# Optimization experiments

Measured on AMD Instinct MI355X. Metric: run time of the kernel, lower is better.

The kernel has to match this reference:

```python
import jax, jax.numpy as jnp
import numpy as np

EMB = 1024
HEADS = 16
EPS = 1e-6


def setup_inputs() -> dict:
    key = jax.random.key(0)
    ks = jax.random.split(key, 12)
    B, S, D = 2, 2048, EMB
    scale = 1.0 / np.sqrt(D)
    inp = {
        "v": jax.random.normal(ks[0], (B, S, D), jnp.float32),
        "k": jax.random.normal(ks[1], (B, S, D), jnp.float32),
        "q": jax.random.normal(ks[2], (B, S, D), jnp.float32),
        "Wv": jax.random.normal(ks[3], (D, D), jnp.float32) * scale,
        "bv": jnp.zeros((D,), jnp.float32),
        "Wk": jax.random.normal(ks[4], (D, D), jnp.float32) * scale,
        "bk": jnp.zeros((D,), jnp.float32),
        "Wq": jax.random.normal(ks[5], (D, D), jnp.float32) * scale,
        "bq": jnp.zeros((D,), jnp.float32),
        "Wo": jax.random.normal(ks[6], (D, D), jnp.float32) * scale,
        "bo": jnp.zeros((D,), jnp.float32),
        "gamma": jnp.ones((D,), jnp.float32),
        "beta": jnp.zeros((D,), jnp.float32),
    }
    return inp


def reference(v, k, q, Wv, bv, Wk, bk, Wq, bq, Wo, bo, gamma, beta):
    B, S, D = q.shape
    H = HEADS
    d = D // H  # head depth

    def split_heads(x):  # [B,S,D] -> [B,H,S,d]
        return x.reshape(B, S, H, d).transpose(0, 2, 1, 3)

    V = split_heads(v @ Wv + bv)
    K = split_heads(k @ Wk + bk)
    Q = split_heads(q @ Wq + bq)

    # scaled dot-product attention (full score matrix, no mask)
    scores = jnp.einsum("bhqd,bhkd->bhqk", Q, K) / jnp.sqrt(jnp.float32(d))
    attn = jax.nn.softmax(scores, axis=-1)
    ctx = jnp.einsum("bhqk,bhkd->bhqd", attn, V)

    ctx = ctx.transpose(0, 2, 1, 3).reshape(B, S, D)
    out = ctx @ Wo + bo + q  # final dense + residual

    # LayerNormalization(epsilon=1e-6) over last axis
    mu = jnp.mean(out, axis=-1, keepdims=True)
    var = jnp.var(out, axis=-1, keepdims=True)
    return gamma * (out - mu) * jax.lax.rsqrt(var + EPS) + beta
```

## Files before the change

kernel.cpp:

```cpp
#include <hip/hip_runtime.h>
#include <hip/hip_bf16.h>
#include <math.h>

#define D_EMB 1024
#define NBATCH 2
#define SEQ 2048
#define NH 16
#define HDIM 64
#define MTOT (NBATCH*SEQ)

typedef unsigned short u16;
typedef __attribute__((ext_vector_type(8))) short bf16x8;
typedef __attribute__((ext_vector_type(4))) float f32x4;
typedef __attribute__((ext_vector_type(16))) float f32x16;
typedef __attribute__((ext_vector_type(4))) unsigned short u16x4;
typedef __attribute__((ext_vector_type(4))) unsigned int u32x4;

__device__ __forceinline__ u16 f2b(float f) {
  union { float f; unsigned u; } x; x.f = f;
  unsigned r = x.u + 0x7fffu + ((x.u >> 16) & 1u);
  return (u16)(r >> 16);
}

__device__ __forceinline__ void gld_lds16(const u16* g, u16* l) {
  __builtin_amdgcn_global_load_lds(
      (const __attribute__((address_space(1))) void*)g,
      (__attribute__((address_space(3))) void*)l, 16, 0, 0);
}

__global__ __launch_bounds__(256) void convert_qkv(
    const float* __restrict__ v, const float* __restrict__ k, const float* __restrict__ q,
    u16* __restrict__ vb, u16* __restrict__ kb, u16* __restrict__ qb) {
  int idx = blockIdx.x * 256 + threadIdx.x;
  float4 a;
  u16x4 o;
  a = ((const float4*)v)[idx];
  o.x = f2b(a.x); o.y = f2b(a.y); o.z = f2b(a.z); o.w = f2b(a.w);
  ((u16x4*)vb)[idx] = o;
  a = ((const float4*)k)[idx];
  o.x = f2b(a.x); o.y = f2b(a.y); o.z = f2b(a.z); o.w = f2b(a.w);
  ((u16x4*)kb)[idx] = o;
  a = ((const float4*)q)[idx];
  o.x = f2b(a.x); o.y = f2b(a.y); o.z = f2b(a.z); o.w = f2b(a.w);
  ((u16x4*)qb)[idx] = o;
}

__global__ __launch_bounds__(256) void transpose_w(
    const float* __restrict__ Wv, const float* __restrict__ Wk,
    const float* __restrict__ Wq, const float* __restrict__ Wo,
    u16* __restrict__ Wvt, u16* __restrict__ Wkt,
    u16* __restrict__ Wqt, u16* __restrict__ Wot) {
  __shared__ float tile[32][33];
  int z = blockIdx.z;
  const float* W = (z==0) ? Wv : (z==1) ? Wk : (z==2) ? Wq : Wo;
  u16* Wt = (z==0) ? Wvt : (z==1) ? Wkt : (z==2) ? Wqt : Wot;
  int tx = threadIdx.x, ty = threadIdx.y;
  int n0 = blockIdx.x * 32, k0 = blockIdx.y * 32;
#pragma unroll
  for (int i = 0; i < 4; ++i)
    tile[ty + i*8][tx] = W[(size_t)(k0 + ty + i*8) * D_EMB + n0 + tx];
  __syncthreads();
#pragma unroll
  for (int i = 0; i < 4; ++i)
    Wt[(size_t)(n0 + ty + i*8) * D_EMB + k0 + tx] = f2b(tile[tx][ty + i*8]);
}

__device__ __forceinline__ void gemm_loop(
    const u16* __restrict__ A, const u16* __restrict__ Bt,
    u16* lds_a, u16* lds_b, int bm, int bn, int wid, int lane,
    int wr, int wc, f32x4 acc[4][4]) {
#pragma unroll 1
  for (int kt = 0; kt < D_EMB/64; ++kt) {
    __syncthreads();
#pragma unroll
    for (int i = 0; i < 4; ++i) {
      int chunk = i*4 + wid;
      int row = chunk*8 + (lane >> 3);
      int slot = (lane & 7) ^ (row & 7);
      const u16* srcA = A + (size_t)(bm*128 + row) * D_EMB + kt*64 + slot*8;
      gld_lds16(srcA, lds_a + chunk*512);
      const u16* srcB = Bt + (size_t)(bn*128 + row) * D_EMB + kt*64 + slot*8;
      gld_lds16(srcB, lds_b + chunk*512);
    }
    __syncthreads();
#pragma unroll
    for (int st = 0; st < 2; ++st) {
      bf16x8 af[4], bfr[4];
#pragma unroll
      for (int mb = 0; mb < 4; ++mb) {
        int row = wr*64 + mb*16 + (lane & 15);
        int slot = (st*4 + (lane >> 4)) ^ (row & 7);
        af[mb] = *(const bf16x8*)(lds_a + row*64 + slot*8);
      }
#pragma unroll
      for (int nb = 0; nb < 4; ++nb) {
        int row = wc*64 + nb*16 + (lane & 15);
        int slot = (st*4 + (lane >> 4)) ^ (row & 7);
        bfr[nb] = *(const bf16x8*)(lds_b + row*64 + slot*8);
      }
#pragma unroll
      for (int mb = 0; mb < 4; ++mb)
#pragma unroll
        for (int nb = 0; nb < 4; ++nb)
          acc[mb][nb] = __builtin_amdgcn_mfma_f32_16x16x32_bf16(af[mb], bfr[nb], acc[mb][nb], 0, 0, 0);
    }
  }
}

__global__ __launch_bounds__(256) void gemm_qkv(
    const u16* __restrict__ vb, const u16* __restrict__ kb, const u16* __restrict__ qb,
    const u16* __restrict__ Wvt, const u16* __restrict__ Wkt, const u16* __restrict__ Wqt,
    const float* __restrict__ bv, const float* __restrict__ bk, const float* __restrict__ bq,
    u16* __restrict__ Vt, u16* __restrict__ Kh, u16* __restrict__ Qh) {
  __shared__ u16 lds_a[128*64];
  __shared__ u16 lds_b[128*64];
  int z = blockIdx.z;
  const u16* A  = (z==0) ? vb : (z==1) ? kb : qb;
  const u16* Bt = (z==0) ? Wvt : (z==1) ? Wkt : Wqt;
  const float* bias = (z==0) ? bv : (z==1) ? bk : bq;
  int tid = threadIdx.x, wid = tid >> 6, lane = tid & 63;
  int wr = wid >> 1, wc = wid & 1;
  int bm = blockIdx.y, bn = blockIdx.x;
  f32x4 acc[4][4];
#pragma unroll
  for (int i = 0; i < 4; ++i)
#pragma unroll
    for (int j = 0; j < 4; ++j) acc[i][j] = (f32x4){0.f,0.f,0.f,0.f};
  gemm_loop(A, Bt, lds_a, lds_b, bm, bn, wid, lane, wr, wc, acc);
  int g = lane >> 4, c = lane & 15;
#pragma unroll
  for (int mb = 0; mb < 4; ++mb) {
    int row0 = bm*128 + wr*64 + mb*16 + g*4;
#pragma unroll
    for (int nb = 0; nb < 4; ++nb) {
      int col = bn*128 + wc*64 + nb*16 + c;
      float bsv = bias[col];
      int h = col >> 6, dd = col & 63;
      if (z == 2) {
#pragma unroll
        for (int r = 0; r < 4; ++r) {
          int m = row0 + r; int b = m >> 11, s = m & (SEQ-1);
          float val = (acc[mb][nb][r] + bsv) * 0.18033688f;
          Qh[(((size_t)b*NH + h)*SEQ + s)*HDIM + dd] = f2b(val);
        }
      } else if (z == 1) {
#pragma unroll
        for (int r = 0; r < 4; ++r) {
          int m = row0 + r; int b = m >> 11, s = m & (SEQ-1);
          Kh[(((size_t)b*NH + h)*SEQ + s)*HDIM + dd] = f2b(acc[mb][nb][r] + bsv);
        }
      } else {
        int m = row0; int b = m >> 11, s = m & (SEQ-1);
        u16x4 pk;
        pk.x = f2b(acc[mb][nb][0] + bsv);
        pk.y = f2b(acc[mb][nb][1] + bsv);
        pk.z = f2b(acc[mb][nb][2] + bsv);
        pk.w = f2b(acc[mb][nb][3] + bsv);
        *(u16x4*)(Vt + (((size_t)b*NH + h)*HDIM + dd)*SEQ + s) = pk;
      }
    }
  }
}

__global__ __launch_bounds__(256, 2) void attn_k(
    const u16* __restrict__ Qh, const u16* __restrict__ Kh,
    const u16* __restrict__ Vt, u16* __restrict__ ctx) {
  __shared__ u16 kt_lds[2][64*64];
  __shared__ u16 vt_lds[2][64*64];
  const int tid = threadIdx.x, wid = tid >> 6, lane = tid & 63;
  const int lo5 = lane & 31, hi = lane >> 5;
  const int bh = blockIdx.y;
  const int qb = blockIdx.x * 128 + wid * 32;
  const size_t base = (size_t)bh * SEQ * HDIM;

  const int srow = tid >> 3;
  const int c0 = (tid & 7) ^ (srow & 7) ^ (srow >> 3);
  const int c1 = c0 ^ 4;
  const u16* kp0 = Kh + base + (size_t)srow * HDIM + c0*8;
  const u16* kp1 = Kh + base + (size_t)(srow+32) * HDIM + c1*8;
  const u16* vp0 = Vt + base + (size_t)srow * SEQ + c0*8;
  const u16* vp1 = Vt + base + (size_t)(srow+32) * SEQ + c1*8;

  const int r7 = lo5 & 7, r3 = lo5 >> 3;
  int offs0[4], offs1[4];
#pragma unroll
  for (int t = 0; t < 4; ++t) {
    int p = (2*t + hi) ^ r7 ^ r3;
    offs0[t] = lo5*128 + p*16;
    offs1[t] = (lo5+32)*128 + (p^4)*16;
  }
  const char* ktbase = (const char*)&kt_lds[0][0];
  const char* vtbase = (const char*)&vt_lds[0][0];

  bf16x8 qf[4];
#pragma unroll
  for (int t = 0; t < 4; ++t)
    qf[t] = *(const bf16x8*)(Qh + base + (size_t)(qb + lo5)*HDIM + t*16 + hi*8);

  bf16x8 onesf;
#pragma unroll
  for (int j = 0; j < 8; ++j) onesf[j] = (short)0x3F80;
  f32x16 z16;
#pragma unroll
  for (int i = 0; i < 16; ++i) z16[i] = 0.f;

  f32x16 o0, o1, lacc;
#pragma unroll
  for (int i = 0; i < 16; ++i) { o0[i] = 0.f; o1[i] = 0.f; lacc[i] = 0.f; }
  float m = -1e30f;
  const float THR = 11.5f;

#define STAGE(B) do { \
    gld_lds16(kp0, &kt_lds[B][wid*512]); \
    gld_lds16(kp1, &kt_lds[B][2048 + wid*512]); \
    gld_lds16(vp0, &vt_lds[B][wid*512]); \
    gld_lds16(vp1, &vt_lds[B][2048 + wid*512]); \
    kp0 += 64*HDIM; kp1 += 64*HDIM; vp0 += 64; vp1 += 64; \
  } while (0)

#define COMPUTE(B) do { \
    const char* kb_ = ktbase + (B)*8192; \
    const char* vb_ = vtbase + (B)*8192; \
    bf16x8 kf0[4], kf1[4]; \
    _Pragma("unroll") for (int t = 0; t < 4; ++t) { \
      kf0[t] = *(const bf16x8*)(kb_ + offs0[t]); \
      kf1[t] = *(const bf16x8*)(kb_ + offs1[t]); } \
    __builtin_amdgcn_s_setprio(1); \
    f32x16 st0 = __builtin_amdgcn_mfma_f32_32x32x16_bf16(kf0[0], qf[0], z16, 0, 0, 0); \
    f32x16 st1 = __builtin_amdgcn_mfma_f32_32x32x16_bf16(kf1[0], qf[0], z16, 0, 0, 0); \
    _Pragma("unroll") for (int t = 1; t < 4; ++t) { \
      st0 = __builtin_amdgcn_mfma_f32_32x32x16_bf16(kf0[t], qf[t], st0, 0, 0, 0); \
      st1 = __builtin_amdgcn_mfma_f32_32x32x16_bf16(kf1[t], qf[t], st1, 0, 0, 0); } \
    __builtin_amdgcn_s_setprio(0); \
    bf16x8 vf0[4], vf1[4]; \
    _Pragma("unroll") for (int t = 0; t < 4; ++t) { \
      vf0[t] = *(const bf16x8*)(vb_ + offs0[t]); \
      vf1[t] = *(const bf16x8*)(vb_ + offs1[t]); } \
    float pm = fmaxf(st0[0], st0[1]); \
    _Pragma("unroll") for (int r = 2; r < 16; r += 2) \
      pm = fmaxf(fmaxf(pm, st0[r]), st0[r+1]); \
    _Pragma("unroll") for (int r = 0; r < 16; r += 2) \
      pm = fmaxf(fmaxf(pm, st1[r]), st1[r+1]); \
    pm = fmaxf(pm, __shfl_xor(pm, 32)); \
    if (__any(pm > m + THR)) { \
      float mn = fmaxf(m, pm); \
      float scl = exp2f(m - mn); \
      m = mn; \
      _Pragma("unroll") for (int r = 0; r < 16; ++r) { \
        int crow = (r & 3) + 8*(r >> 2) + 4*hi; \
        float sr = __int_as_float( \
            __builtin_amdgcn_ds_bpermute(crow << 2, __float_as_int(scl))); \
        o0[r] *= sr; o1[r] *= sr; lacc[r] *= sr; } } \
    _Pragma("unroll") for (int r = 0; r < 16; ++r) st0[r] = exp2f(st0[r] - m); \
    _Pragma("unroll") for (int r = 0; r < 16; ++r) st1[r] = exp2f(st1[r] - m); \
    bf16x8 pa[4]; \
    _Pragma("unroll") for (int ks = 0; ks < 2; ++ks) { \
      const f32x16& s_ = ks ? st1 : st0; \
      unsigned X[8]; \
      _Pragma("unroll") for (int w = 0; w < 8; ++w) { \
        float lo_f = s_[2*w], hi_f = s_[2*w + 1]; \
        asm("v_cvt_pk_bf16_f32 %0, %1, %2" : "=v"(X[w]) : "v"(lo_f), "v"(hi_f)); } \
      asm volatile("v_permlane32_swap_b32 %0, %1" : "+v"(X[0]), "+v"(X[2])); \
      asm volatile("v_permlane32_swap_b32 %0, %1" : "+v"(X[1]), "+v"(X[3])); \
      asm volatile("v_permlane32_swap_b32 %0, %1" : "+v"(X[4]), "+v"(X[6])); \
      asm volatile("v_permlane32_swap_b32 %0, %1" : "+v"(X[5]), "+v"(X[7])); \
      union { u32x4 u; bf16x8 b; } cva, cvb; \
      cva.u = (u32x4){X[0], X[1], X[2], X[3]}; \
      cvb.u = (u32x4){X[4], X[5], X[6], X[7]}; \
      pa[2*ks]   = cva.b; \
      pa[2*ks+1] = cvb.b; } \
    __builtin_amdgcn_s_setprio(1); \
    _Pragma("unroll") for (int t = 0; t < 4; ++t) { \
      o0 = __builtin_amdgcn_mfma_f32_32x32x16_bf16(pa[t], vf0[t], o0, 0, 0, 0); \
      o1 = __builtin_amdgcn_mfma_f32_32x32x16_bf16(pa[t], vf1[t], o1, 0, 0, 0); } \
    _Pragma("unroll") for (int t = 0; t < 4; ++t) \
      lacc = __builtin_amdgcn_mfma_f32_32x32x16_bf16(pa[t], onesf, lacc, 0, 0, 0); \
    __builtin_amdgcn_s_setprio(0); \
  } while (0)

  STAGE(0);
  asm volatile("s_waitcnt vmcnt(0)");
  __syncthreads();

#pragma unroll 1
  for (int kv = 0; kv < SEQ/64 - 2; kv += 2) {
    STAGE(1);
    COMPUTE(0);
    asm volatile("s_waitcnt vmcnt(0)");
    __syncthreads();
    STAGE(0);
    COMPUTE(1);
    asm volatile("s_waitcnt vmcnt(0)");
    __syncthreads();
  }
  STAGE(1);
  COMPUTE(0);
  asm volatile("s_waitcnt vmcnt(0)");
  __syncthreads();
  COMPUTE(1);

#undef STAGE
#undef COMPUTE

  const int b = bh >> 4, h = bh & 15;
#pragma unroll
  for (int r = 0; r < 16; ++r) {
    int crow = (r & 3) + 8*(r >> 2) + 4*hi;
    float lr = 1.0f / lacc[r];
    int s = qb + crow;
    u16* row = ctx + ((size_t)(b*SEQ + s))*D_EMB + h*64;
    row[lo5]      = f2b(o0[r] * lr);
    row[32 + lo5] = f2b(o1[r] * lr);
  }
}

__global__ __launch_bounds__(256) void gemm_out(
    const u16* __restrict__ ctx, const u16* __restrict__ Wot,
    const float* __restrict__ bo, const float* __restrict__ resid,
    float* __restrict__ preln) {
  __shared__ u16 lds_a[128*64];
  __shared__ u16 lds_b[128*64];
  int tid = threadIdx.x, wid = tid >> 6, lane = tid & 63;
  int wr = wid >> 1, wc = wid & 1;
  int bm = blockIdx.y, bn = blockIdx.x;
  f32x4 acc[4][4];
#pragma unroll
  for (int i = 0; i < 4; ++i)
#pragma unroll
    for (int j = 0; j < 4; ++j) acc[i][j] = (f32x4){0.f,0.f,0.f,0.f};
  gemm_loop(ctx, Wot, lds_a, lds_b, bm, bn, wid, lane, wr, wc, acc);
  int g = lane >> 4, c = lane & 15;
#pragma unroll
  for (int mb = 0; mb < 4; ++mb) {
    int row0 = bm*128 + wr*64 + mb*16 + g*4;
#pragma unroll
    for (int nb = 0; nb < 4; ++nb) {
      int col = bn*128 + wc*64 + nb*16 + c;
      float bsv = bo[col];
#pragma unroll
      for (int r = 0; r < 4; ++r) {
        int m = row0 + r;
        preln[(size_t)m*D_EMB + col] = acc[mb][nb][r] + bsv + resid[(size_t)m*D_EMB + col];
      }
    }
  }
}

__global__ __launch_bounds__(256) void ln_k(
    const float* __restrict__ preln, const float* __restrict__ gamma,
    const float* __restrict__ beta, float* __restrict__ out) {
  int row = blockIdx.x, tid = threadIdx.x;
  float4 x = ((const float4*)(preln + (size_t)row*D_EMB))[tid];
  float s  = x.x + x.y + x.z + x.w;
  float ss = x.x*x.x + x.y*x.y + x.z*x.z + x.w*x.w;
#pragma unroll
  for (int off = 32; off; off >>= 1) {
    s  += __shfl_xor(s, off);
    ss += __shfl_xor(ss, off);
  }
  __shared__ float red_s[4], red_ss[4];
  int wid = tid >> 6, lane = tid & 63;
  if (lane == 0) { red_s[wid] = s; red_ss[wid] = ss; }
  __syncthreads();
  s  = red_s[0] + red_s[1] + red_s[2] + red_s[3];
  ss = red_ss[0] + red_ss[1] + red_ss[2] + red_ss[3];
  float mu = s * (1.0f/1024.0f);
  float var = ss * (1.0f/1024.0f) - mu*mu;
  float rstd = rsqrtf(var + 1e-6f);
  float4 gm = ((const float4*)gamma)[tid];
  float4 bt = ((const float4*)beta)[tid];
  float4 y;
  y.x = (x.x - mu)*rstd*gm.x + bt.x;
  y.y = (x.y - mu)*rstd*gm.y + bt.y;
  y.z = (x.z - mu)*rstd*gm.z + bt.z;
  y.w = (x.w - mu)*rstd*gm.w + bt.w;
  ((float4*)(out + (size_t)row*D_EMB))[tid] = y;
}

extern "C" void kernel_launch(void* const* d_in, const int* in_sizes, int n_in,
                              void* d_out, int out_size, void* d_ws, size_t ws_size,
                              hipStream_t stream) {
  const float* v_in  = (const float*)d_in[0];
  const float* k_in  = (const float*)d_in[1];
  const float* q_in  = (const float*)d_in[2];
  const float* Wv    = (const float*)d_in[3];
  const float* bv    = (const float*)d_in[4];
  const float* Wk    = (const float*)d_in[5];
  const float* bk    = (const float*)d_in[6];
  const float* Wq    = (const float*)d_in[7];
  const float* bq    = (const float*)d_in[8];
  const float* Wo    = (const float*)d_in[9];
  const float* bo    = (const float*)d_in[10];
  const float* gamma = (const float*)d_in[11];
  const float* beta  = (const float*)d_in[12];
  char* ws = (char*)d_ws;

  const size_t TOKB = (size_t)MTOT * D_EMB * 2;
  const size_t WB   = (size_t)D_EMB * D_EMB * 2;
  size_t o_qb = 0;
  size_t o_kb = o_qb + TOKB;
  size_t o_vb = o_kb + TOKB;
  size_t o_wq = o_vb + TOKB;
  size_t o_wk = o_wq + WB;
  size_t o_wv = o_wk + WB;
  size_t o_wo = o_wv + WB;
  size_t o_Qh = o_wo + WB;
  size_t o_Kh = o_Qh + TOKB;
  size_t o_Vt = o_Kh + TOKB;
  size_t o_cx = o_Vt + TOKB;

  u16* qb  = (u16*)(ws + o_qb);
  u16* kb  = (u16*)(ws + o_kb);
  u16* vb  = (u16*)(ws + o_vb);
  u16* wqt = (u16*)(ws + o_wq);
  u16* wkt = (u16*)(ws + o_wk);
  u16* wvt = (u16*)(ws + o_wv);
  u16* wot = (u16*)(ws + o_wo);
  u16* Qh  = (u16*)(ws + o_Qh);
  u16* Kh  = (u16*)(ws + o_Kh);
  u16* Vt  = (u16*)(ws + o_Vt);
  u16* cx  = (u16*)(ws + o_cx);
  float* preln = (float*)(ws + 0);

  convert_qkv<<<4096, 256, 0, stream>>>(v_in, k_in, q_in, vb, kb, qb);
  transpose_w<<<dim3(32, 32, 4), dim3(32, 8), 0, stream>>>(Wv, Wk, Wq, Wo, wvt, wkt, wqt, wot);
  gemm_qkv<<<dim3(8, 32, 3), 256, 0, stream>>>(vb, kb, qb, wvt, wkt, wqt, bv, bk, bq, Vt, Kh, Qh);
  attn_k<<<dim3(16, 32), 256, 0, stream>>>(Qh, Kh, Vt, cx);
  gemm_out<<<dim3(8, 32), 256, 0, stream>>>(cx, wot, bo, q_in, preln);
  ln_k<<<4096, 256, 0, stream>>>(preln, gamma, beta, (float*)d_out);
}
```

Measured before the change: 159.9 us.

## Split attention over KV halves with a separate combine kernel

Splits the attention key/value sequence into two halves across a third grid dimension, so each block processes 16 KV tiles instead of 32. Each block writes unnormalized bf16 partial outputs plus its running max and row sum, and a new combine kernel merges the two halves with rescaling before gemm_out. Launch bounds are raised to 4 blocks per SM for more occupancy. The intent is to raise parallelism from 512 blocks to 1024 on a 256-CU device. The cost is an extra kernel launch, extra global traffic for partials, and extra bf16 rounding of the unnormalized partials.

```diff
diff --git a/kernel.cpp b/kernel.cpp
--- a/kernel.cpp
+++ b/kernel.cpp
@@ -8,6 +8,8 @@
 #define NH 16
 #define HDIM 64
 #define MTOT (NBATCH*SEQ)
+#define NSPLIT 2
+#define NT_SPLIT 16
 
 typedef unsigned short u16;
 typedef __attribute__((ext_vector_type(8))) short bf16x8;
@@ -20,6 +22,10 @@
   union { float f; unsigned u; } x; x.f = f;
   unsigned r = x.u + 0x7fffu + ((x.u >> 16) & 1u);
   return (u16)(r >> 16);
+}
+__device__ __forceinline__ float b2f(u16 u) {
+  union { unsigned u; float f; } x; x.u = ((unsigned)u) << 16;
+  return x.f;
 }
 
 __device__ __forceinline__ void gld_lds16(const u16* g, u16* l) {
@@ -162,24 +168,26 @@
   }
 }
 
-__global__ __launch_bounds__(256, 2) void attn_k(
+__global__ __launch_bounds__(256, 4) void attn_k(
     const u16* __restrict__ Qh, const u16* __restrict__ Kh,
-    const u16* __restrict__ Vt, u16* __restrict__ ctx) {
+    const u16* __restrict__ Vt, u16* __restrict__ Opart,
+    float* __restrict__ Lm, float* __restrict__ Ll) {
   __shared__ u16 kt_lds[2][64*64];
   __shared__ u16 vt_lds[2][64*64];
   const int tid = threadIdx.x, wid = tid >> 6, lane = tid & 63;
   const int lo5 = lane & 31, hi = lane >> 5;
-  const int bh = blockIdx.y;
+  const int bh = blockIdx.y, sp = blockIdx.z;
   const int qb = blockIdx.x * 128 + wid * 32;
   const size_t base = (size_t)bh * SEQ * HDIM;
 
   const int srow = tid >> 3;
   const int c0 = (tid & 7) ^ (srow & 7) ^ (srow >> 3);
   const int c1 = c0 ^ 4;
-  const u16* kp0 = Kh + base + (size_t)srow * HDIM + c0*8;
-  const u16* kp1 = Kh + base + (size_t)(srow+32) * HDIM + c1*8;
-  const u16* vp0 = Vt + base + (size_t)srow * SEQ + c0*8;
-  const u16* vp1 = Vt + base + (size_t)(srow+32) * SEQ + c1*8;
+  const u16* kp0 = Kh + base + (size_t)(sp*NT_SPLIT*64 + srow) * HDIM + c0*8;
+  const u16* kp1 = kp0 + 32*HDIM;
+  const u16* vp0 = Vt + base + (size_t)srow * SEQ + sp*NT_SPLIT*64 + c0*8;
+  const u16* vp1 = Vt + base + (size_t)(srow+32) * SEQ + sp*NT_SPLIT*64 + c1*8;
+  kp1 = Kh + base + (size_t)(sp*NT_SPLIT*64 + srow + 32) * HDIM + c1*8;
 
   const int r7 = lo5 & 7, r3 = lo5 >> 3;
   int offs0[4], offs1[4];
@@ -236,11 +244,13 @@
     _Pragma("unroll") for (int t = 0; t < 4; ++t) { \
       vf0[t] = *(const bf16x8*)(vb_ + offs0[t]); \
       vf1[t] = *(const bf16x8*)(vb_ + offs1[t]); } \
-    float pm = fmaxf(st0[0], st0[1]); \
-    _Pragma("unroll") for (int r = 2; r < 16; r += 2) \
-      pm = fmaxf(fmaxf(pm, st0[r]), st0[r+1]); \
-    _Pragma("unroll") for (int r = 0; r < 16; r += 2) \
-      pm = fmaxf(fmaxf(pm, st1[r]), st1[r+1]); \
+    float pm = fmaxf(fmaxf(st0[0], st0[1]), st0[2]); \
+    _Pragma("unroll") for (int r = 3; r < 15; r += 3) \
+      pm = fmaxf(fmaxf(fmaxf(pm, st0[r]), st0[r+1]), st0[r+2]); \
+    pm = fmaxf(pm, st0[15]); \
+    _Pragma("unroll") for (int r = 0; r < 15; r += 3) \
+      pm = fmaxf(fmaxf(fmaxf(pm, st1[r]), st1[r+1]), st1[r+2]); \
+    pm = fmaxf(pm, st1[15]); \
     pm = fmaxf(pm, __shfl_xor(pm, 32)); \
     if (__any(pm > m + THR)) { \
       float mn = fmaxf(m, pm); \
@@ -283,7 +293,7 @@
   __syncthreads();
 
 #pragma unroll 1
-  for (int kv = 0; kv < SEQ/64 - 2; kv += 2) {
+  for (int kv = 0; kv < NT_SPLIT - 2; kv += 2) {
     STAGE(1);
     COMPUTE(0);
     asm volatile("s_waitcnt vmcnt(0)");
@@ -302,16 +312,57 @@
 #undef STAGE
 #undef COMPUTE
 
-  const int b = bh >> 4, h = bh & 15;
+  const int prow0 = (sp*32 + bh) * SEQ + qb;
 #pragma unroll
   for (int r = 0; r < 16; ++r) {
     int crow = (r & 3) + 8*(r >> 2) + 4*hi;
-    float lr = 1.0f / lacc[r];
-    int s = qb + crow;
-    u16* row = ctx + ((size_t)(b*SEQ + s))*D_EMB + h*64;
-    row[lo5]      = f2b(o0[r] * lr);
-    row[32 + lo5] = f2b(o1[r] * lr);
-  }
+    u16* row = Opart + (size_t)(prow0 + crow)*HDIM;
+    row[lo5]      = f2b(o0[r]);
+    row[32 + lo5] = f2b(o1[r]);
+  }
+  if (hi == 0) Lm[prow0 + lo5] = m;
+  if (lo5 == 0) {
+#pragma unroll
+    for (int r = 0; r < 16; ++r) {
+      int crow = (r & 3) + 8*(r >> 2) + 4*hi;
+      Ll[prow0 + crow] = lacc[r];
+    }
+  }
+}
+
+__global__ __launch_bounds__(256) void combine_k(
+    const u16* __restrict__ Opart, const float* __restrict__ Lm,
+    const float* __restrict__ Ll, u16* __restrict__ ctx) {
+  int gid = blockIdx.x * 256 + threadIdx.x;
+  int row = gid >> 2;
+  int dseg = (gid & 3) << 4;
+  const int STRROW = 32 * SEQ;
+  float m1 = Lm[row], m2 = Lm[STRROW + row];
+  float l1 = Ll[row], l2 = Ll[STRROW + row];
+  float ms = fmaxf(m1, m2);
+  float w1 = exp2f(m1 - ms), w2 = exp2f(m2 - ms);
+  float inv = 1.0f / (w1*l1 + w2*l2);
+  w1 *= inv; w2 *= inv;
+  const u16* p1 = Opart + (size_t)row*HDIM + dseg;
+  const u16* p2 = p1 + (size_t)STRROW*HDIM;
+  bf16x8 a0 = *(const bf16x8*)p1, a1 = *(const bf16x8*)(p1 + 8);
+  bf16x8 b0 = *(const bf16x8*)p2, b1 = *(const bf16x8*)(p2 + 8);
+  int bh = row >> 11, s = row & (SEQ-1);
+  int b = bh >> 4, h = bh & 15;
+  u16* dst = ctx + ((size_t)(b*SEQ + s))*D_EMB + h*64 + dseg;
+  u16x4 o[4];
+#pragma unroll
+  for (int j = 0; j < 8; ++j) {
+    float f = w1*b2f((u16)a0[j]) + w2*b2f((u16)b0[j]);
+    ((u16*)o)[j] = f2b(f);
+  }
+#pragma unroll
+  for (int j = 0; j < 8; ++j) {
+    float f = w1*b2f((u16)a1[j]) + w2*b2f((u16)b1[j]);
+    ((u16*)o)[8 + j] = f2b(f);
+  }
+#pragma unroll
+  for (int j = 0; j < 4; ++j) ((u16x4*)dst)[j] = o[j];
 }
 
 __global__ __launch_bounds__(256) void gemm_out(
@@ -420,12 +471,16 @@
   u16* Kh  = (u16*)(ws + o_Kh);
   u16* Vt  = (u16*)(ws + o_Vt);
   u16* cx  = (u16*)(ws + o_cx);
+  u16* Opart = (u16*)(ws + 0);
+  float* Lm  = (float*)(ws + 2*TOKB);
+  float* Ll  = (float*)(ws + 2*TOKB + NSPLIT*32*SEQ*4);
   float* preln = (float*)(ws + 0);
 
   convert_qkv<<<4096, 256, 0, stream>>>(v_in, k_in, q_in, vb, kb, qb);
   transpose_w<<<dim3(32, 32, 4), dim3(32, 8), 0, stream>>>(Wv, Wk, Wq, Wo, wvt, wkt, wqt, wot);
   gemm_qkv<<<dim3(8, 32, 3), 256, 0, stream>>>(vb, kb, qb, wvt, wkt, wqt, bv, bk, bq, Vt, Kh, Qh);
-  attn_k<<<dim3(16, 32), 256, 0, stream>>>(Qh, Kh, Vt, cx);
+  attn_k<<<dim3(16, 32, NSPLIT), 256, 0, stream>>>(Qh, Kh, Vt, Opart, Lm, Ll);
+  combine_k<<<1024, 256, 0, stream>>>(Opart, Lm, Ll, cx);
   gemm_out<<<dim3(8, 32), 256, 0, stream>>>(cx, wot, bo, q_in, preln);
   ln_k<<<4096, 256, 0, stream>>>(preln, gamma, beta, (float*)d_out);
 }
```

Result: slower. 441.9 us (+176.5%).

## Deepen attention K/V prefetch pipeline with partial vmcnt waits and early LDS reads

Applied to the files above, without the earlier changes.

Restructures the flash-attention inner loop so two K/V tiles are in flight. Each tile waits only for its own loads (vmcnt(4)), reads both K and V fragments from LDS up front, then barriers and issues the next stage into the freed buffer before the MFMAs. This removes the full vmcnt(0) drain per tile and hides global-load latency behind compute. It also reshapes the row-max reduction into 3-input max chains. The cost is more live registers for the V fragments and an extra barrier per tile.

```diff
diff --git a/kernel.cpp b/kernel.cpp
--- a/kernel.cpp
+++ b/kernel.cpp
@@ -8,6 +8,7 @@
 #define NH 16
 #define HDIM 64
 #define MTOT (NBATCH*SEQ)
+#define NT (SEQ/64)
 
 typedef unsigned short u16;
 typedef __attribute__((ext_vector_type(8))) short bf16x8;
@@ -218,13 +219,25 @@
     kp0 += 64*HDIM; kp1 += 64*HDIM; vp0 += 64; vp1 += 64; \
   } while (0)
 
-#define COMPUTE(B) do { \
+#define TILE(B, VMSTR, DOSTAGE) do { \
+    asm volatile("s_waitcnt " VMSTR ::: "memory"); \
+    __builtin_amdgcn_sched_barrier(0); \
+    __builtin_amdgcn_s_barrier();             \
+    __builtin_amdgcn_sched_barrier(0); \
     const char* kb_ = ktbase + (B)*8192; \
     const char* vb_ = vtbase + (B)*8192; \
-    bf16x8 kf0[4], kf1[4]; \
+    bf16x8 kf0[4], kf1[4], vf0[4], vf1[4]; \
     _Pragma("unroll") for (int t = 0; t < 4; ++t) { \
       kf0[t] = *(const bf16x8*)(kb_ + offs0[t]); \
-      kf1[t] = *(const bf16x8*)(kb_ + offs1[t]); } \
+      kf1[t] = *(const bf16x8*)(kb_ + offs1[t]); \
+      vf0[t] = *(const bf16x8*)(vb_ + offs0[t]); \
+      vf1[t] = *(const bf16x8*)(vb_ + offs1[t]); } \
+    asm volatile("s_waitcnt lgkmcnt(0)" ::: "memory"); \
+    __builtin_amdgcn_sched_barrier(0); \
+    __builtin_amdgcn_s_barrier();             \
+    __builtin_amdgcn_sched_barrier(0); \
+    if (DOSTAGE) { STAGE(B); } \
+    __builtin_amdgcn_sched_barrier(0); \
     __builtin_amdgcn_s_setprio(1); \
     f32x16 st0 = __builtin_amdgcn_mfma_f32_32x32x16_bf16(kf0[0], qf[0], z16, 0, 0, 0); \
     f32x16 st1 = __builtin_amdgcn_mfma_f32_32x32x16_bf16(kf1[0], qf[0], z16, 0, 0, 0); \
@@ -232,15 +245,13 @@
       st0 = __builtin_amdgcn_mfma_f32_32x32x16_bf16(kf0[t], qf[t], st0, 0, 0, 0); \
       st1 = __builtin_amdgcn_mfma_f32_32x32x16_bf16(kf1[t], qf[t], st1, 0, 0, 0); } \
     __builtin_amdgcn_s_setprio(0); \
-    bf16x8 vf0[4], vf1[4]; \
-    _Pragma("unroll") for (int t = 0; t < 4; ++t) { \
-      vf0[t] = *(const bf16x8*)(vb_ + offs0[t]); \
-      vf1[t] = *(const bf16x8*)(vb_ + offs1[t]); } \
-    float pm = fmaxf(st0[0], st0[1]); \
-    _Pragma("unroll") for (int r = 2; r < 16; r += 2) \
-      pm = fmaxf(fmaxf(pm, st0[r]), st0[r+1]); \
-    _Pragma("unroll") for (int r = 0; r < 16; r += 2) \
-      pm = fmaxf(fmaxf(pm, st1[r]), st1[r+1]); \
+    float pm = fmaxf(fmaxf(st0[0], st0[1]), st0[2]); \
+    _Pragma("unroll") for (int r = 3; r < 15; r += 3) \
+      pm = fmaxf(fmaxf(fmaxf(pm, st0[r]), st0[r+1]), st0[r+2]); \
+    pm = fmaxf(pm, st0[15]); \
+    _Pragma("unroll") for (int r = 0; r < 15; r += 3) \
+      pm = fmaxf(fmaxf(fmaxf(pm, st1[r]), st1[r+1]), st1[r+2]); \
+    pm = fmaxf(pm, st1[15]); \
     pm = fmaxf(pm, __shfl_xor(pm, 32)); \
     if (__any(pm > m + THR)) { \
       float mn = fmaxf(m, pm); \
@@ -279,28 +290,18 @@
   } while (0)
 
   STAGE(0);
-  asm volatile("s_waitcnt vmcnt(0)");
-  __syncthreads();
+  STAGE(1);
 
 #pragma unroll 1
-  for (int kv = 0; kv < SEQ/64 - 2; kv += 2) {
-    STAGE(1);
-    COMPUTE(0);
-    asm volatile("s_waitcnt vmcnt(0)");
-    __syncthreads();
-    STAGE(0);
-    COMPUTE(1);
-    asm volatile("s_waitcnt vmcnt(0)");
-    __syncthreads();
-  }
-  STAGE(1);
-  COMPUTE(0);
-  asm volatile("s_waitcnt vmcnt(0)");
-  __syncthreads();
-  COMPUTE(1);
+  for (int kv = 0; kv < NT - 2; kv += 2) {
+    TILE(0, "vmcnt(4)", 1);
+    TILE(1, "vmcnt(4)", 1);
+  }
+  TILE(0, "vmcnt(4)", 0);
+  TILE(1, "vmcnt(0)", 0);
 
 #undef STAGE
-#undef COMPUTE
+#undef TILE
 
   const int b = bh >> 4, h = bh & 15;
 #pragma unroll
```

New measurement: 159.2 us. About the same (-0.4%).
